# Kernel tuning notes

Measured on AMD Instinct MI355X. Metric: run time of the kernel, lower is better.

The kernel has to match this reference:

```python
import jax, jax.numpy as jnp
import numpy as np
import math

N_HEAD = 16


def setup_inputs() -> dict:
    key = jax.random.key(0)
    ks = jax.random.split(key, 5)
    B, T, C = 2, 2048, 2048
    x = jax.random.normal(ks[0], (B, T, C), dtype=jnp.float32)
    # additive causal mask: 0 on/below diagonal, large negative above
    causal = jnp.tril(jnp.ones((T, T), dtype=bool))
    attention_mask = jnp.where(causal, 0.0, -1e9).astype(jnp.float32)[None, None]
    scale = 0.02
    W_attn = jax.random.normal(ks[1], (C, 3 * C), dtype=jnp.float32) * scale
    b_attn = jax.random.normal(ks[2], (3 * C,), dtype=jnp.float32) * scale
    W_proj = jax.random.normal(ks[3], (C, C), dtype=jnp.float32) * scale
    b_proj = jax.random.normal(ks[4], (C,), dtype=jnp.float32) * scale
    return {"x": x, "attention_mask": attention_mask, "W_attn": W_attn,
            "b_attn": b_attn, "W_proj": W_proj, "b_proj": b_proj}


def reference(x, attention_mask, W_attn, b_attn, W_proj, b_proj):
    B, T, C = x.shape
    H = N_HEAD
    Dh = C // H
    qkv = x @ W_attn + b_attn                      # [B,T,3C]
    q, k, v = jnp.split(qkv, 3, axis=2)            # each [B,T,C]
    current_cache = jnp.concatenate([k, v], axis=2)  # [B,T,2C]
    qh = q.reshape(B, T, H, Dh).transpose(0, 2, 1, 3)  # [B,H,T,Dh]
    kh = k.reshape(B, T, H, Dh).transpose(0, 2, 1, 3)
    vh = v.reshape(B, T, H, Dh).transpose(0, 2, 1, 3)
    att = jnp.einsum('bhqd,bhkd->bhqk', qh, kh) * (1.0 / math.sqrt(Dh))
    att = att + attention_mask                     # broadcast [1,1,T,T]
    att = jax.nn.softmax(att, axis=-1)
    y = jnp.einsum('bhqk,bhkd->bhqd', att, vh)     # [B,H,T,Dh]
    y = y.transpose(0, 2, 1, 3).reshape(B, T, C)
    y = y @ W_proj + b_proj                        # [B,T,C]
    return (y, current_cache)
```

## Files before the change

### kernel.cpp

```cpp
#include <hip/hip_runtime.h>

typedef __attribute__((ext_vector_type(8))) short bf16x8;
typedef __attribute__((ext_vector_type(4))) float f32x4;

#define MFMA16(a, b, c) __builtin_amdgcn_mfma_f32_16x16x32_bf16((a), (b), (c), 0, 0, 0)

static __device__ __forceinline__ short f2bf(float f) {
  unsigned u = __builtin_bit_cast(unsigned, f);
  unsigned r = (u + 0x7FFFu + ((u >> 16) & 1u)) >> 16;
  return (short)(unsigned short)r;
}
static __device__ __forceinline__ unsigned pack2(float lo, float hi) {
  return (unsigned)(unsigned short)f2bf(lo) | ((unsigned)(unsigned short)f2bf(hi) << 16);
}

static __device__ __forceinline__ void glds16(const void* g, void* l) {
  __builtin_amdgcn_global_load_lds((const __attribute__((address_space(1))) unsigned*)g,
                                   (__attribute__((address_space(3))) unsigned*)l, 16, 0, 0);
}

__global__ __launch_bounds__(256) void prep_kernel(const float* __restrict__ x,
                                                   short* __restrict__ x_bf,
                                                   const float* __restrict__ W_attn,
                                                   short* __restrict__ wt_attn,
                                                   const float* __restrict__ W_proj,
                                                   short* __restrict__ wt_proj) {
  __shared__ float tile[64][65];
  int bid = blockIdx.x;
  if (bid < 4096) {
    size_t i = ((size_t)bid * 256 + threadIdx.x) * 8;
    float4 a = *(const float4*)(x + i);
    float4 b = *(const float4*)(x + i + 4);
    uint4 o;
    o.x = pack2(a.x, a.y);
    o.y = pack2(a.z, a.w);
    o.z = pack2(b.x, b.y);
    o.w = pack2(b.z, b.w);
    *(uint4*)(x_bf + i) = o;
    return;
  }
  const float* in;
  short* out;
  int R = 2048, Cc, r0, c0;
  if (bid < 7168) {
    int r = bid - 4096;
    in = W_attn; out = wt_attn; Cc = 6144;
    c0 = (r % 96) * 64; r0 = (r / 96) * 64;
  } else {
    int r = bid - 7168;
    in = W_proj; out = wt_proj; Cc = 2048;
    c0 = (r & 31) * 64; r0 = (r >> 5) * 64;
  }
  int tx = threadIdx.x & 15, ty = threadIdx.x >> 4;
#pragma unroll
  for (int i = 0; i < 4; i++) {
    int r = ty + i * 16;
    float4 v = *(const float4*)(in + (size_t)(r0 + r) * Cc + c0 + tx * 4);
    tile[r][tx * 4 + 0] = v.x;
    tile[r][tx * 4 + 1] = v.y;
    tile[r][tx * 4 + 2] = v.z;
    tile[r][tx * 4 + 3] = v.w;
  }
  __syncthreads();
#pragma unroll
  for (int i = 0; i < 4; i++) {
    int co = ty + i * 16;
    uint2 o;
    o.x = pack2(tile[tx * 4 + 0][co], tile[tx * 4 + 1][co]);
    o.y = pack2(tile[tx * 4 + 2][co], tile[tx * 4 + 3][co]);
    *(uint2*)(out + (size_t)(c0 + co) * R + r0 + tx * 4) = o;
  }
}


#define AFQ(C, KS, MT) (*(const bf16x8*)&lds[(C)*16384 + (KS)*8192 + (wr4 + (MT)) * 512 + rdoff])
#define BFQ(C, KS, NT) \
  (*(const bf16x8*)&lds[32768 + (C)*8192 + (KS)*4096 + (wc4 + (NT)) * 512 + rdoff])

#define STAGE(C, KS, KT)                                                           \
  do {                                                                             \
    glds16(Asrc0 + (KT) * 64 + (KS) * 32, &lds[(C)*16384 + (KS)*8192 + wid * 512]); \
    glds16(Asrc1 + (KT) * 64 + (KS) * 32,                                          \
           &lds[(C)*16384 + (KS)*8192 + (wid + 8) * 512]);                         \
    glds16(Bsrc0 + (KT) * 64 + (KS) * 32,                                          \
           &lds[32768 + (C)*8192 + (KS)*4096 + wid * 512]);                        \
  } while (0)

#define MIDBAR                                                       \
  do {                                                               \
    asm volatile("s_barrier\n\ts_waitcnt lgkmcnt(0)" ::: "memory");  \
    __builtin_amdgcn_sched_barrier(0);                               \
  } while (0)
#define ENDBARV6                                                     \
  do {                                                               \
    __builtin_amdgcn_sched_barrier(0);                               \
    asm volatile("s_waitcnt vmcnt(6)\n\ts_barrier" ::: "memory");    \
    __builtin_amdgcn_sched_barrier(0);                               \
  } while (0)

#define MMROW(AR, MT)                            \
  do {                                           \
    acc[MT][0] = MFMA16(AR, bfr[0], acc[MT][0]); \
    acc[MT][1] = MFMA16(AR, bfr[1], acc[MT][1]); \
    acc[MT][2] = MFMA16(AR, bfr[2], acc[MT][2]); \
    acc[MT][3] = MFMA16(AR, bfr[3], acc[MT][3]); \
  } while (0)

#define PHASE(C, KS, STG)          \
  do {                             \
    af[0] = AFQ(C, KS, 0);         \
    af[1] = AFQ(C, KS, 1);         \
    af[2] = AFQ(C, KS, 2);         \
    af[3] = AFQ(C, KS, 3);         \
    bfr[0] = BFQ(C, KS, 0);        \
    bfr[1] = BFQ(C, KS, 1);        \
    bfr[2] = BFQ(C, KS, 2);        \
    bfr[3] = BFQ(C, KS, 3);        \
    STG;                           \
    MIDBAR;                        \
    __builtin_amdgcn_s_setprio(1); \
    MMROW(af[0], 0);               \
    MMROW(af[1], 1);               \
    MMROW(af[2], 2);               \
    MMROW(af[3], 3);               \
    __builtin_amdgcn_s_setprio(0); \
    ENDBARV6;                      \
  } while (0)

#define KTILE(C, NX, MM)                     \
  do {                                       \
    int s1 = (MM) + 1 > 31 ? 31 : (MM) + 1;  \
    int s2 = (MM) + 2 > 31 ? 31 : (MM) + 2;  \
    PHASE(C, 0, STAGE(NX, 1, s1));           \
    PHASE(C, 1, STAGE(C, 0, s2));            \
  } while (0)

#define GEMM_PREAMBLE(Aptr, Bptr)                                                  \
  __shared__ __align__(16) short lds[49152];                           \
  int tid = threadIdx.x;                                                           \
  int lane = tid & 63, wid = tid >> 6;                                             \
  int l15 = lane & 15, l4 = lane >> 4;                                             \
  int wr = wid >> 1, wc = wid & 1;                                                 \
  int wr4 = wr * 4, wc4 = wc * 4;                                                  \
  int wprime = (lane * 16) ^ (lane & 32);                                          \
  int r_ = wprime >> 6;                                                            \
  int cs_ = (wprime & 63) >> 1;                                                    \
  const short* Asrc0 = (Aptr) + (size_t)(rowBase + wid * 16 + r_) * 2048 + cs_;    \
  const short* Asrc1 = (Aptr) + (size_t)(rowBase + (wid + 8) * 16 + r_) * 2048 + cs_; \
  const short* Bsrc0 = (Bptr) + (size_t)(colBase + wid * 16 + r_) * 2048 + cs_;    \
  int rdoff = l15 * 32 + ((l4 * 8) ^ ((l15 & 8) << 1));                            \
  f32x4 zero = {0.f, 0.f, 0.f, 0.f};                                               \
  f32x4 acc[4][4];                                                                 \
  _Pragma("unroll") for (int i = 0; i < 4; i++) _Pragma("unroll") for (int j = 0;  \
                                                                       j < 4; j++) \
      acc[i][j] = zero;                                                            \
  bf16x8 af[4], bfr[4];                                                            \
  STAGE(0, 0, 0);                                                                  \
  STAGE(0, 1, 0);                                                                  \
  STAGE(1, 0, 1);                                                                  \
  asm volatile("s_waitcnt vmcnt(6)" ::: "memory");                                 \
  __builtin_amdgcn_sched_barrier(0);                                               \
  asm volatile("s_barrier" ::: "memory");                                          \
  __builtin_amdgcn_sched_barrier(0);                                               \
  for (int it = 0; it < 16; ++it) {                                                \
    int m0 = it * 2;                                                               \
    KTILE(0, 1, m0);                                                               \
    KTILE(1, 0, m0 + 1);                                                           \
  }                                                                                \
  asm volatile("s_waitcnt vmcnt(0)" ::: "memory");                                 \
  __syncthreads();

__global__ __launch_bounds__(512, 2) void gemm_qkv_kernel(const short* __restrict__ A,
                                                          const short* __restrict__ Bt,
                                                          const float* __restrict__ bias,
                                                          short* __restrict__ q_bf,
                                                          short* __restrict__ k_bf,
                                                          short* __restrict__ vt,
                                                          float* __restrict__ cache) {
  int bid = blockIdx.x;
  int s = (bid & 7) * 96 + (bid >> 3);
  int bx = s % 48, by = s / 48;
  int rowBase = by * 256, colBase = bx * 128;

  GEMM_PREAMBLE(A, Bt)

  int seg = colBase >> 11;
  int colLoc = colBase & 2047;
  float scale = (seg == 0) ? 0.08838834764831845f : 1.0f;
  float bv[4];
#pragma unroll
  for (int nt = 0; nt < 4; nt++) bv[nt] = bias[colBase + wc * 64 + nt * 16 + l15];

  short(*Cs)[136] = (short(*)[136])lds;
#pragma unroll
  for (int mt = 0; mt < 4; mt++)
#pragma unroll
    for (int nt = 0; nt < 4; nt++)
#pragma unroll
      for (int r = 0; r < 4; r++)
        Cs[wr * 64 + mt * 16 + l4 * 4 + r][wc * 64 + nt * 16 + l15] =
            f2bf((acc[mt][nt][r] + bv[nt]) * scale);
  __syncthreads();

  if (seg < 2) {
    short* outp = (seg == 0) ? q_bf : k_bf;
#pragma unroll
    for (int pp = 0; pp < 8; pp++) {
      int idx = pp * 512 + tid;
      int row = idx >> 4, c8 = (idx & 15) * 8;
      *(uint4*)(outp + (size_t)(rowBase + row) * 2048 + colLoc + c8) =
          *(const uint4*)&Cs[row][c8];
    }
  } else {
    int b_ = rowBase >> 11, rowLoc = rowBase & 2047;
    int hh = colLoc >> 7;
    short* vrow = vt + (size_t)((b_ * 16 + hh) * 128) * 2048;
    int tx = tid & 7, dbase = tid >> 3;
#pragma unroll
    for (int dd = 0; dd < 2; dd++) {
      int d = dbase + dd * 64;
#pragma unroll
      for (int g = 0; g < 4; g++) {
        short tmp[8];
#pragma unroll
        for (int j = 0; j < 8; j++) {
          int p = tx * 8 + j;
          int tl = (p & 32) + ((p & 1) << 4) + ((p >> 1) & 15);
          tmp[j] = Cs[g * 64 + tl][d];
        }
        *(uint4*)(vrow + (size_t)d * 2048 + rowLoc + g * 64 + tx * 8) = *(uint4*)tmp;
      }
    }
  }

  if (seg) {
    int coff = (seg == 1) ? 0 : 2048;
#pragma unroll
    for (int mt = 0; mt < 4; mt++)
#pragma unroll
      for (int nt = 0; nt < 4; nt++) {
        int cc = coff + colLoc + wc * 64 + nt * 16 + l15;
#pragma unroll
        for (int r = 0; r < 4; r++) {
          int row = rowBase + wr * 64 + mt * 16 + l4 * 4 + r;
          cache[(size_t)row * 4096 + cc] = acc[mt][nt][r] + bv[nt];
        }
      }
  }
}

__global__ __launch_bounds__(512, 2) void gemm_proj_kernel(const short* __restrict__ A,
                                                           const short* __restrict__ Bt,
                                                           const float* __restrict__ bias,
                                                           float* __restrict__ out_y) {
  int bid = blockIdx.x;
  int s = (bid & 7) * 32 + (bid >> 3);
  int bx = s % 16, by = s / 16;
  int rowBase = by * 256, colBase = bx * 128;

  GEMM_PREAMBLE(A, Bt)

#pragma unroll
  for (int mt = 0; mt < 4; mt++)
#pragma unroll
    for (int nt = 0; nt < 4; nt++) {
      int col = colBase + wc * 64 + nt * 16 + l15;
      float bvv = bias[col];
#pragma unroll
      for (int r = 0; r < 4; r++) {
        int row = rowBase + wr * 64 + mt * 16 + l4 * 4 + r;
        out_y[(size_t)row * 2048 + col] = acc[mt][nt][r] + bvv;
      }
    }
}

#define LDK 136
#define LDV 72
#define LDP 72

__global__ __launch_bounds__(512, 2) void attn_kernel(const short* __restrict__ qb,
                                                      const short* __restrict__ kb,
                                                      const short* __restrict__ vtb,
                                                      short* __restrict__ attout) {
  __shared__ short Ks[64 * LDK];
  __shared__ short Vs[128 * LDV];
  __shared__ short Ps[8][32 * LDP];

  int tid = threadIdx.x;
  int lane = tid & 63, wid = tid >> 6;
  int l15 = lane & 15, l4 = lane >> 4;
  int qlo = blockIdx.x, qhi = 15 - qlo;
  int h = blockIdx.y, b = blockIdx.z;
  int myqt = (wid < 4) ? qhi : qlo;
  int qrow0 = myqt * 128 + (wid & 3) * 32;
  int kdiag = qrow0 >> 6;
  int ktmax = 2 * qhi + 1;
  size_t qkbase = (size_t)b * 2048 * 2048 + (size_t)h * 128;
  size_t vbase = (size_t)((b * 16 + h) * 128) * 2048;

  bf16x8 qf[2][4];
#pragma unroll
  for (int m = 0; m < 2; m++)
#pragma unroll
    for (int kk = 0; kk < 4; kk++)
      qf[m][kk] =
          *(const bf16x8*)(qb + qkbase + (size_t)(qrow0 + m * 16 + l15) * 2048 + kk * 32 + l4 * 8);

  short onev = (short)0x3F80;
  bf16x8 ones = {onev, onev, onev, onev, onev, onev, onev, onev};

  f32x4 zero = {0.f, 0.f, 0.f, 0.f};
  f32x4 o[2][8], ol[2];
#pragma unroll
  for (int m = 0; m < 2; m++) {
#pragma unroll
    for (int n = 0; n < 8; n++) o[m][n] = zero;
    ol[m] = zero;
  }

  int c0 = tid, c1 = 512 + tid;
  int kr0 = c0 >> 4, kc0 = (c0 & 15) * 8;
  int kr1 = c1 >> 4, kc1 = (c1 & 15) * 8;
  int dr0 = c0 >> 3, tc0 = (c0 & 7) * 8;
  int dr1 = c1 >> 3, tc1 = (c1 & 7) * 8;
  const short* kA = kb + qkbase + (size_t)kr0 * 2048 + kc0;
  const short* kB = kb + qkbase + (size_t)kr1 * 2048 + kc1;
  const short* vA = vtb + vbase + (size_t)dr0 * 2048 + tc0;
  const short* vB = vtb + vbase + (size_t)dr1 * 2048 + tc1;

  uint4 krg0 = *(const uint4*)kA;
  uint4 krg1 = *(const uint4*)kB;
  uint4 vrg0 = *(const uint4*)vA;
  uint4 vrg1 = *(const uint4*)vB;

  for (int kt = 0; kt <= ktmax; kt++) {
    __syncthreads();
    *(uint4*)&Ks[kr0 * LDK + kc0] = krg0;
    *(uint4*)&Ks[kr1 * LDK + kc1] = krg1;
    *(uint4*)&Vs[dr0 * LDV + tc0] = vrg0;
    *(uint4*)&Vs[dr1 * LDV + tc1] = vrg1;
    if (kt < ktmax) {
      size_t ko = (size_t)(kt + 1) * 64 * 2048;
      int vo = (kt + 1) * 64;
      krg0 = *(const uint4*)(kA + ko);
      krg1 = *(const uint4*)(kB + ko);
      vrg0 = *(const uint4*)(vA + vo);
      vrg1 = *(const uint4*)(vB + vo);
    }
    __syncthreads();

    if (kt <= kdiag) {
      f32x4 s[2][4];
#pragma unroll
      for (int m = 0; m < 2; m++)
#pragma unroll
        for (int nt = 0; nt < 4; nt++) s[m][nt] = zero;
#pragma unroll
      for (int kk = 0; kk < 4; kk++) {
#pragma unroll
        for (int nt = 0; nt < 4; nt++) {
          bf16x8 kf = *(const bf16x8*)&Ks[(nt * 16 + l15) * LDK + kk * 32 + l4 * 8];
          s[0][nt] = MFMA16(qf[0][kk], kf, s[0][nt]);
          s[1][nt] = MFMA16(qf[1][kk], kf, s[1][nt]);
        }
      }

      if (kt == kdiag) {
        int kt0 = kt * 64;
#pragma unroll
        for (int m = 0; m < 2; m++)
#pragma unroll
          for (int nt = 0; nt < 4; nt++) {
            int colg = kt0 + nt * 16 + l15;
#pragma unroll
            for (int r = 0; r < 4; r++) {
              int rowg = qrow0 + m * 16 + l4 * 4 + r;
              if (colg > rowg) s[m][nt][r] = -1e30f;
            }
          }
      }

#pragma unroll
      for (int m = 0; m < 2; m++)
#pragma unroll
        for (int r = 0; r < 4; r++) {
          float p0 = __expf(s[m][0][r]);
          float p1 = __expf(s[m][1][r]);
          float p2 = __expf(s[m][2][r]);
          float p3 = __expf(s[m][3][r]);
          int prow = (m * 16 + l4 * 4 + r) * LDP;
          *(unsigned*)&Ps[wid][prow + 2 * l15] = pack2(p0, p1);
          *(unsigned*)&Ps[wid][prow + 32 + 2 * l15] = pack2(p2, p3);
        }

#pragma unroll
      for (int kk = 0; kk < 2; kk++) {
        bf16x8 pf0 = *(const bf16x8*)&Ps[wid][l15 * LDP + kk * 32 + l4 * 8];
        bf16x8 pf1 = *(const bf16x8*)&Ps[wid][(16 + l15) * LDP + kk * 32 + l4 * 8];
        ol[0] = MFMA16(pf0, ones, ol[0]);
        ol[1] = MFMA16(pf1, ones, ol[1]);
#pragma unroll
        for (int n = 0; n < 8; n++) {
          bf16x8 vf = *(const bf16x8*)&Vs[(n * 16 + l15) * LDV + kk * 32 + l4 * 8];
          o[0][n] = MFMA16(pf0, vf, o[0][n]);
          o[1][n] = MFMA16(pf1, vf, o[1][n]);
        }
      }
    }
  }

#pragma unroll
  for (int m = 0; m < 2; m++) {
    float rl[4];
#pragma unroll
    for (int r = 0; r < 4; r++) rl[r] = 1.0f / ol[m][r];
#pragma unroll
    for (int n = 0; n < 8; n++)
#pragma unroll
      for (int r = 0; r < 4; r++)
        attout[qkbase + (size_t)(qrow0 + m * 16 + l4 * 4 + r) * 2048 + n * 16 + l15] =
            f2bf(o[m][n][r] * rl[r]);
  }
}

extern "C" void kernel_launch(void* const* d_in, const int* in_sizes, int n_in, void* d_out,
                              int out_size, void* d_ws, size_t ws_size, hipStream_t stream) {
  const float* x = (const float*)d_in[0];
  const float* W_attn = (const float*)d_in[2];
  const float* b_attn = (const float*)d_in[3];
  const float* W_proj = (const float*)d_in[4];
  const float* b_proj = (const float*)d_in[5];
  float* y = (float*)d_out;
  float* cache = y + (size_t)4096 * 2048;

  char* p = (char*)d_ws;
  short* x_bf = (short*)p;   p += (size_t)8388608 * 2;
  short* q_bf = (short*)p;   p += (size_t)8388608 * 2;
  short* k_bf = (short*)p;   p += (size_t)8388608 * 2;
  short* vt_bf = (short*)p;  p += (size_t)8388608 * 2;
  short* att_bf = (short*)p; p += (size_t)8388608 * 2;
  short* wt_attn = (short*)p; p += (size_t)12582912 * 2;
  short* wt_proj = (short*)p; p += (size_t)4194304 * 2;

  prep_kernel<<<8192, 256, 0, stream>>>(x, x_bf, W_attn, wt_attn, W_proj, wt_proj);
  gemm_qkv_kernel<<<768, 512, 0, stream>>>(x_bf, wt_attn, b_attn, q_bf, k_bf, vt_bf, cache);
  attn_kernel<<<dim3(8, 16, 2), 512, 0, stream>>>(q_bf, k_bf, vt_bf, att_bf);
  gemm_proj_kernel<<<256, 512, 0, stream>>>(att_bf, wt_proj, b_proj, y);
}
```

Baseline: 396.7 us.

## Switch GEMM mainloop to triple-buffered full 64-wide K tiles per phase

```diff
diff --git a/kernel.cpp b/kernel.cpp
--- a/kernel.cpp
+++ b/kernel.cpp
@@ -73,17 +73,20 @@
 }
 
 
-#define AFQ(C, KS, MT) (*(const bf16x8*)&lds[(C)*16384 + (KS)*8192 + (wr4 + (MT)) * 512 + rdoff])
-#define BFQ(C, KS, NT) \
-  (*(const bf16x8*)&lds[32768 + (C)*8192 + (KS)*4096 + (wc4 + (NT)) * 512 + rdoff])
-
-#define STAGE(C, KS, KT)                                                           \
-  do {                                                                             \
-    glds16(Asrc0 + (KT) * 64 + (KS) * 32, &lds[(C)*16384 + (KS)*8192 + wid * 512]); \
-    glds16(Asrc1 + (KT) * 64 + (KS) * 32,                                          \
-           &lds[(C)*16384 + (KS)*8192 + (wid + 8) * 512]);                         \
-    glds16(Bsrc0 + (KT) * 64 + (KS) * 32,                                          \
-           &lds[32768 + (C)*8192 + (KS)*4096 + wid * 512]);                        \
+#define AFQ3(C, KS, MT) \
+  (*(const bf16x8*)&lds[(C)*24576 + (KS)*8192 + (wr4 + (MT)) * 512 + rdoff])
+#define BFQ3(C, KS, NT) \
+  (*(const bf16x8*)&lds[(C)*24576 + 16384 + (KS)*4096 + (wc4 + (NT)) * 512 + rdoff])
+
+#define STAGE3(C, KT)                                                     \
+  do {                                                                    \
+    glds16(Asrc0 + (KT) * 64, &lds[(C)*24576 + wid * 512]);               \
+    glds16(Asrc1 + (KT) * 64, &lds[(C)*24576 + (wid + 8) * 512]);         \
+    glds16(Asrc0 + (KT) * 64 + 32, &lds[(C)*24576 + 8192 + wid * 512]);   \
+    glds16(Asrc1 + (KT) * 64 + 32,                                        \
+           &lds[(C)*24576 + 8192 + (wid + 8) * 512]);                     \
+    glds16(Bsrc0 + (KT) * 64, &lds[(C)*24576 + 16384 + wid * 512]);       \
+    glds16(Bsrc0 + (KT) * 64 + 32, &lds[(C)*24576 + 20480 + wid * 512]);  \
   } while (0)
 
 #define MIDBAR                                                       \
@@ -98,45 +101,49 @@
     __builtin_amdgcn_sched_barrier(0);                               \
   } while (0)
 
-#define MMROW(AR, MT)                            \
-  do {                                           \
-    acc[MT][0] = MFMA16(AR, bfr[0], acc[MT][0]); \
-    acc[MT][1] = MFMA16(AR, bfr[1], acc[MT][1]); \
-    acc[MT][2] = MFMA16(AR, bfr[2], acc[MT][2]); \
-    acc[MT][3] = MFMA16(AR, bfr[3], acc[MT][3]); \
+#define MMROW(AR, BV, MT)                            \
+  do {                                               \
+    acc[MT][0] = MFMA16(AR, BV[0], acc[MT][0]);      \
+    acc[MT][1] = MFMA16(AR, BV[1], acc[MT][1]);      \
+    acc[MT][2] = MFMA16(AR, BV[2], acc[MT][2]);      \
+    acc[MT][3] = MFMA16(AR, BV[3], acc[MT][3]);      \
   } while (0)
 
-#define PHASE(C, KS, STG)          \
+#define PHASE64(C, CN, KT)         \
   do {                             \
-    af[0] = AFQ(C, KS, 0);         \
-    af[1] = AFQ(C, KS, 1);         \
-    af[2] = AFQ(C, KS, 2);         \
-    af[3] = AFQ(C, KS, 3);         \
-    bfr[0] = BFQ(C, KS, 0);        \
-    bfr[1] = BFQ(C, KS, 1);        \
-    bfr[2] = BFQ(C, KS, 2);        \
-    bfr[3] = BFQ(C, KS, 3);        \
-    STG;                           \
+    af[0] = AFQ3(C, 0, 0);         \
+    af[1] = AFQ3(C, 0, 1);         \
+    af[2] = AFQ3(C, 0, 2);         \
+    af[3] = AFQ3(C, 0, 3);         \
+    bfr[0] = BFQ3(C, 0, 0);        \
+    bfr[1] = BFQ3(C, 0, 1);        \
+    bfr[2] = BFQ3(C, 0, 2);        \
+    bfr[3] = BFQ3(C, 0, 3);        \
+    ag[0] = AFQ3(C, 1, 0);         \
+    ag[1] = AFQ3(C, 1, 1);         \
+    ag[2] = AFQ3(C, 1, 2);         \
+    ag[3] = AFQ3(C, 1, 3);         \
+    bg[0] = BFQ3(C, 1, 0);         \
+    bg[1] = BFQ3(C, 1, 1);         \
+    bg[2] = BFQ3(C, 1, 2);         \
+    bg[3] = BFQ3(C, 1, 3);         \
+    STAGE3(CN, KT);                \
     MIDBAR;                        \
     __builtin_amdgcn_s_setprio(1); \
-    MMROW(af[0], 0);               \
-    MMROW(af[1], 1);               \
-    MMROW(af[2], 2);               \
-    MMROW(af[3], 3);               \
+    MMROW(af[0], bfr, 0);          \
+    MMROW(af[1], bfr, 1);          \
+    MMROW(af[2], bfr, 2);          \
+    MMROW(af[3], bfr, 3);          \
+    MMROW(ag[0], bg, 0);           \
+    MMROW(ag[1], bg, 1);           \
+    MMROW(ag[2], bg, 2);           \
+    MMROW(ag[3], bg, 3);           \
     __builtin_amdgcn_s_setprio(0); \
     ENDBARV6;                      \
   } while (0)
 
-#define KTILE(C, NX, MM)                     \
-  do {                                       \
-    int s1 = (MM) + 1 > 31 ? 31 : (MM) + 1;  \
-    int s2 = (MM) + 2 > 31 ? 31 : (MM) + 2;  \
-    PHASE(C, 0, STAGE(NX, 1, s1));           \
-    PHASE(C, 1, STAGE(C, 0, s2));            \
-  } while (0)
-
 #define GEMM_PREAMBLE(Aptr, Bptr)                                                  \
-  __shared__ __align__(16) short lds[49152];                           \
+  __shared__ __align__(16) short lds[73728];                          \
   int tid = threadIdx.x;                                                           \
   int lane = tid & 63, wid = tid >> 6;                                             \
   int l15 = lane & 15, l4 = lane >> 4;                                             \
@@ -154,19 +161,20 @@
   _Pragma("unroll") for (int i = 0; i < 4; i++) _Pragma("unroll") for (int j = 0;  \
                                                                        j < 4; j++) \
       acc[i][j] = zero;                                                            \
-  bf16x8 af[4], bfr[4];                                                            \
-  STAGE(0, 0, 0);                                                                  \
-  STAGE(0, 1, 0);                                                                  \
-  STAGE(1, 0, 1);                                                                  \
+  bf16x8 af[4], bfr[4], ag[4], bg[4];                                              \
+  STAGE3(0, 0);                                                                    \
+  STAGE3(1, 1);                                                                    \
   asm volatile("s_waitcnt vmcnt(6)" ::: "memory");                                 \
   __builtin_amdgcn_sched_barrier(0);                                               \
   asm volatile("s_barrier" ::: "memory");                                          \
   __builtin_amdgcn_sched_barrier(0);                                               \
-  for (int it = 0; it < 16; ++it) {                                                \
-    int m0 = it * 2;                                                               \
-    KTILE(0, 1, m0);                                                               \
-    KTILE(1, 0, m0 + 1);                                                           \
+  for (int t = 0; t < 30; t += 3) {                                                \
+    PHASE64(0, 2, t + 2);                                                          \
+    PHASE64(1, 0, t + 3);                                                          \
+    PHASE64(2, 1, t + 4);                                                          \
   }                                                                                \
+  PHASE64(0, 2, 31);           \
+  PHASE64(1, 0, 31);                                  \
   asm volatile("s_waitcnt vmcnt(0)" ::: "memory");                                 \
   __syncthreads();
 
```

New measurement: 407.0 us. 2.6% more time.
